# Kernel tuning notes

Measured on AMD Instinct MI355X. Metric: run time of the kernel, lower is better.

## Reference

```python
import jax, jax.numpy as jnp
import numpy as np

N_NODES = 50000
IN_CH = 128
HID = 32
HEADS = 4
OUT_CH = 32
N_EDGES = 1600000
NEG_SLOPE = 0.2


def _gatv2(x, src, dst, Wl, bl, Wr, br, att, bias, H, C):
    """GATv2Conv (PyG semantics, add_self_loops already applied to src/dst).
    x: [N, F_in]; src/dst: [E]; Wl/Wr: [F_in, H*C]; att: [H, C]; bias: [H*C].
    Returns [N, H*C] (concat heads)."""
    N = x.shape[0]
    xl = (x @ Wl + bl).reshape(N, H, C)  # source-side transform
    xr = (x @ Wr + br).reshape(N, H, C)  # target-side transform
    e = jax.nn.leaky_relu(xl[src] + xr[dst], NEG_SLOPE)  # [E, H, C]
    logits = jnp.einsum('ehc,hc->eh', e, att)  # [E, H]
    # softmax over incoming edges of each target node (stable)
    m = jax.ops.segment_max(logits, dst, num_segments=N)[dst]
    p = jnp.exp(logits - m)
    denom = jax.ops.segment_sum(p, dst, num_segments=N)[dst]
    alpha = p / denom  # [E, H]
    out = jax.ops.segment_sum(alpha[:, :, None] * xl[src], dst, num_segments=N)
    return out.reshape(N, H * C) + bias


def setup_inputs() -> dict:
    key = jax.random.key(0)
    ks = jax.random.split(key, 16)
    s1 = 1.0 / np.sqrt(IN_CH)
    s2 = 1.0 / np.sqrt(HID * HEADS)
    inp = {
        'x': jax.random.normal(ks[0], (N_NODES, IN_CH), jnp.float32),
        'edge_index': jax.random.randint(ks[1], (2, N_EDGES), 0, N_NODES, jnp.int64 if jax.config.read('jax_enable_x64') else jnp.int32).astype(jnp.int32),
        # layer 1: in -> HID per head, HEADS heads
        'Wl1': jax.random.normal(ks[2], (IN_CH, HEADS * HID), jnp.float32) * s1,
        'bl1': jnp.zeros((HEADS * HID,), jnp.float32),
        'Wr1': jax.random.normal(ks[3], (IN_CH, HEADS * HID), jnp.float32) * s1,
        'br1': jnp.zeros((HEADS * HID,), jnp.float32),
        'att1': jax.random.normal(ks[4], (HEADS, HID), jnp.float32) * s1,
        'b1': jnp.zeros((HEADS * HID,), jnp.float32),
        # mu head: HID*HEADS -> OUT_CH, 1 head
        'Wl_mu': jax.random.normal(ks[5], (HEADS * HID, OUT_CH), jnp.float32) * s2,
        'bl_mu': jnp.zeros((OUT_CH,), jnp.float32),
        'Wr_mu': jax.random.normal(ks[6], (HEADS * HID, OUT_CH), jnp.float32) * s2,
        'br_mu': jnp.zeros((OUT_CH,), jnp.float32),
        'att_mu': jax.random.normal(ks[7], (1, OUT_CH), jnp.float32) * s2,
        'b_mu': jnp.zeros((OUT_CH,), jnp.float32),
        # logvar head
        'Wl_lv': jax.random.normal(ks[8], (HEADS * HID, OUT_CH), jnp.float32) * s2,
        'bl_lv': jnp.zeros((OUT_CH,), jnp.float32),
        'Wr_lv': jax.random.normal(ks[9], (HEADS * HID, OUT_CH), jnp.float32) * s2,
        'br_lv': jnp.zeros((OUT_CH,), jnp.float32),
        'att_lv': jax.random.normal(ks[10], (1, OUT_CH), jnp.float32) * s2,
        'b_lv': jnp.zeros((OUT_CH,), jnp.float32),
    }
    return inp


def reference(x, edge_index, Wl1, bl1, Wr1, br1, att1, b1,
              Wl_mu, bl_mu, Wr_mu, br_mu, att_mu, b_mu,
              Wl_lv, bl_lv, Wr_lv, br_lv, att_lv, b_lv):
    N = x.shape[0]
    loops = jnp.arange(N, dtype=edge_index.dtype)
    src = jnp.concatenate([edge_index[0], loops])  # add_self_loops=True
    dst = jnp.concatenate([edge_index[1], loops])
    h = jax.nn.relu(_gatv2(x, src, dst, Wl1, bl1, Wr1, br1, att1, b1, HEADS, HID))
    mu = _gatv2(h, src, dst, Wl_mu, bl_mu, Wr_mu, br_mu, att_mu, b_mu, 1, OUT_CH)
    logvar = _gatv2(h, src, dst, Wl_lv, bl_lv, Wr_lv, br_lv, att_lv, b_lv, 1, OUT_CH)
    return (mu, logvar)
```

## Files before the change

kernel.cpp:

```cpp
#include <hip/hip_runtime.h>
#include <hip/hip_fp16.h>

#define NNODES 50000
#define EORIG  1600000
#define ETOT   (EORIG + NNODES)
#define NEG 0.2f
#define BSH 7
#define NBUCK ((NNODES + 127) >> BSH)
#define BCAP 5120
#define NRT (NNODES / 16)
#define EPB 4096
#define NBE ((ETOT + EPB - 1) / EPB)
#define LOG2E 1.44269504f

typedef _Float16 v2h __attribute__((ext_vector_type(2)));
typedef _Float16 v8h __attribute__((ext_vector_type(8)));
typedef float    v4f __attribute__((ext_vector_type(4)));

__device__ __forceinline__ float hdot2v(v2h a, v2h b, float c) {
#if __has_builtin(__builtin_amdgcn_fdot2)
    return __builtin_amdgcn_fdot2(a, b, c, false);
#else
    return c + (float)a.x * (float)b.x + (float)a.y * (float)b.y;
#endif
}

__device__ __forceinline__ float fexp2(float t) {
#if __has_builtin(__builtin_amdgcn_exp2f)
    return __builtin_amdgcn_exp2f(t);
#else
    return exp2f(t);
#endif
}

__global__ __launch_bounds__(256) void prep_kernel(
    const int* __restrict__ src, const int* __restrict__ dst,
    int* __restrict__ bcur, unsigned int* __restrict__ pairs,
    const float* __restrict__ Wl, const float* __restrict__ Wr,
    const float* __restrict__ Wlmu, const float* __restrict__ Wllv,
    const float* __restrict__ Wrmu, const float* __restrict__ Wrlv,
    __half* __restrict__ WT, __half* __restrict__ WT2)
{
    if (blockIdx.x >= NBE) {
        int id = (blockIdx.x - NBE) * 256 + threadIdx.x;
        if (id < 32768) {
            int k = id >> 8, c = id & 255;
            float v = (c < 128) ? Wl[k * 128 + c] : Wr[k * 128 + (c - 128)];
            WT[c * 128 + k] = __float2half(v);
        } else if (id < 49152) {
            int loc = id - 32768;
            int k = loc >> 7, c = loc & 127;
            int sel = c >> 5, cc = c & 31;
            const float* W = sel == 0 ? Wlmu : sel == 1 ? Wllv : sel == 2 ? Wrmu : Wrlv;
            WT2[c * 128 + k] = __float2half(W[k * 32 + cc]);
        }
        return;
    }

    __shared__ int cnt[NBUCK];
    __shared__ int gbase[NBUCK];
    const int e0 = blockIdx.x * EPB;

    for (int i = threadIdx.x; i < NBUCK; i += 256) cnt[i] = 0;
    __syncthreads();

    for (int i = threadIdx.x; i < EPB; i += 256) {
        int e = e0 + i;
        if (e >= ETOT) break;
        int d = (e < EORIG) ? dst[e] : e - EORIG;
        atomicAdd(&cnt[d >> BSH], 1);
    }
    __syncthreads();

    for (int b = threadIdx.x; b < NBUCK; b += 256) {
        int c = cnt[b];
        gbase[b] = c ? (b * BCAP + atomicAdd(&bcur[b], c)) : 0;
        cnt[b] = 0;
    }
    __syncthreads();

    for (int i = threadIdx.x; i < EPB; i += 256) {
        int e = e0 + i;
        if (e >= ETOT) break;
        int s, d;
        if (e < EORIG) { s = src[e]; d = dst[e]; }
        else           { s = d = e - EORIG; }
        int b = d >> BSH;
        int slot = atomicAdd(&cnt[b], 1);
        pairs[gbase[b] + slot] = (unsigned)s | ((unsigned)(d & 127) << 16);
    }
}

__global__ __launch_bounds__(256) void csrfill_kernel(
    const unsigned int* __restrict__ pairs, const int* __restrict__ bcur,
    int2* __restrict__ begend, unsigned short* __restrict__ csr)
{
    __shared__ int cnt[128];
    __shared__ int lofs[128];
    __shared__ int scnt[128];
    const int b = blockIdx.x, n0 = b << BSH;
    const int nn = min(128, NNODES - n0);
    const int pbase = b * BCAP;
    const int pend = pbase + bcur[b];
    const int t = threadIdx.x;

    if (t < 128) { cnt[t] = 0; scnt[t] = 0; }
    __syncthreads();
    for (int i = pbase + t; i < pend; i += 256)
        atomicAdd(&cnt[pairs[i] >> 16], 1);
    __syncthreads();

    int myc = (t < 128) ? cnt[t] : 0;
    if (t < 128) lofs[t] = myc;
    __syncthreads();
    for (int off = 1; off < 128; off <<= 1) {
        int v = (t < 128 && t >= off) ? lofs[t - off] : 0;
        __syncthreads();
        if (t < 128) lofs[t] += v;
        __syncthreads();
    }
    if (t < 128) lofs[t] = pbase + lofs[t] - myc;
    __syncthreads();

    if (t < nn) begend[n0 + t] = make_int2(lofs[t], lofs[t] + myc);

    for (int i = pbase + t; i < pend; i += 256) {
        unsigned pr = pairs[i];
        int l = pr >> 16;
        int slot = atomicAdd(&scnt[l], 1);
        csr[lofs[l] + slot] = (unsigned short)(pr & 0xFFFFu);
    }
}

__global__ __launch_bounds__(256) void lin1_kernel(
    const float* __restrict__ x, const __half* __restrict__ WT,
    const float* __restrict__ bl, const float* __restrict__ br,
    __half* __restrict__ xl16, __half* __restrict__ xr16)
{
    int rt = (blockIdx.x * 256 + threadIdx.x) >> 6;
    if (rt >= NRT) return;
    int l  = threadIdx.x & 63;
    int lr = l & 15, lg = l >> 4;
    int row = rt * 16 + lr;

    v8h a[4];
    const float4* xrow = reinterpret_cast<const float4*>(x + (size_t)row * 128);
    #pragma unroll
    for (int ks = 0; ks < 4; ++ks) {
        float4 f0 = xrow[ks * 8 + lg * 2];
        float4 f1 = xrow[ks * 8 + lg * 2 + 1];
        v8h t;
        t[0]=(_Float16)f0.x; t[1]=(_Float16)f0.y; t[2]=(_Float16)f0.z; t[3]=(_Float16)f0.w;
        t[4]=(_Float16)f1.x; t[5]=(_Float16)f1.y; t[6]=(_Float16)f1.z; t[7]=(_Float16)f1.w;
        a[ks] = t;
    }

    const uint4* wt4 = reinterpret_cast<const uint4*>(WT);
    #pragma unroll 4
    for (int ct = 0; ct < 16; ++ct) {
        int c = ct * 16 + lr;
        v4f acc = {0.f, 0.f, 0.f, 0.f};
        #pragma unroll
        for (int ks = 0; ks < 4; ++ks) {
            union { uint4 u; v8h h; } B;
            B.u = wt4[(size_t)c * 16 + ks * 4 + lg];
            acc = __builtin_amdgcn_mfma_f32_16x16x32_f16(a[ks], B.h, acc, 0, 0, 0);
        }
        float bb = (c < 128) ? bl[c] : br[c - 128];
        #pragma unroll
        for (int j = 0; j < 4; ++j) {
            int orow = rt * 16 + lg * 4 + j;
            __half hv = __float2half(acc[j] + bb);
            if (c < 128) xl16[(size_t)orow * 128 + c] = hv;
            else         xr16[(size_t)orow * 128 + (c - 128)] = hv;
        }
    }
}

__global__ __launch_bounds__(256) void lin2_kernel(
    const __half* __restrict__ h16, const __half* __restrict__ WT2,
    const float* __restrict__ blmu, const float* __restrict__ bllv,
    const float* __restrict__ brmu, const float* __restrict__ brlv,
    __half* __restrict__ xi16, __half* __restrict__ xrI16)
{
    int rt = (blockIdx.x * 256 + threadIdx.x) >> 6;
    if (rt >= NRT) return;
    int l  = threadIdx.x & 63;
    int lr = l & 15, lg = l >> 4;
    int row = rt * 16 + lr;

    v8h a[4];
    const uint4* hrow = reinterpret_cast<const uint4*>(h16 + (size_t)row * 128);
    #pragma unroll
    for (int ks = 0; ks < 4; ++ks) {
        union { uint4 u; v8h h; } A;
        A.u = hrow[ks * 4 + lg];
        a[ks] = A.h;
    }

    const uint4* wt4 = reinterpret_cast<const uint4*>(WT2);
    #pragma unroll 4
    for (int ct = 0; ct < 8; ++ct) {
        int c = ct * 16 + lr;
        v4f acc = {0.f, 0.f, 0.f, 0.f};
        #pragma unroll
        for (int ks = 0; ks < 4; ++ks) {
            union { uint4 u; v8h h; } B;
            B.u = wt4[(size_t)c * 16 + ks * 4 + lg];
            acc = __builtin_amdgcn_mfma_f32_16x16x32_f16(a[ks], B.h, acc, 0, 0, 0);
        }
        int sel = c >> 5, cc = c & 31;
        const float* bp = sel == 0 ? blmu : sel == 1 ? bllv : sel == 2 ? brmu : brlv;
        float bb = bp[cc];
        #pragma unroll
        for (int j = 0; j < 4; ++j) {
            int orow = rt * 16 + lg * 4 + j;
            __half hv = __float2half(acc[j] + bb);
            if (c < 64) xi16 [(size_t)orow * 64 + c]      = hv;
            else        xrI16[(size_t)orow * 64 + (c-64)] = hv;
        }
    }
}

__global__ __launch_bounds__(256) void gat_gather1(
    const __half* __restrict__ xl16, const __half* __restrict__ xr16,
    const float* __restrict__ att, const float* __restrict__ bias,
    const int2* __restrict__ begend, const unsigned short* __restrict__ csr,
    __half* __restrict__ h16)
{
    int d = (blockIdx.x * 256 + threadIdx.x) >> 6;
    if (d >= NNODES) return;
    int lane = threadIdx.x & 63;
    int quarter = lane >> 4;
    int q = lane & 15;
    int qo = quarter * 2;

    v2h xrh[4], ath[4];
    {
        union { uint4 u; v2h v[4]; } R;
        R.u = reinterpret_cast<const uint4*>(xr16)[d * 16 + q];
        #pragma unroll
        for (int j = 0; j < 4; ++j) xrh[j] = R.v[j];
        const float4* t4 = reinterpret_cast<const float4*>(att) + q * 2;
        float4 a = t4[0], b = t4[1];
        ath[0] = (v2h){(_Float16)(a.x*LOG2E), (_Float16)(a.y*LOG2E)};
        ath[1] = (v2h){(_Float16)(a.z*LOG2E), (_Float16)(a.w*LOG2E)};
        ath[2] = (v2h){(_Float16)(b.x*LOG2E), (_Float16)(b.y*LOG2E)};
        ath[3] = (v2h){(_Float16)(b.z*LOG2E), (_Float16)(b.w*LOG2E)};
    }
    const v2h neg2 = (v2h){(_Float16)NEG, (_Float16)NEG};

    int2 be = begend[d];
    int beg = be.x, end = be.y;
    int deg = end - beg;
    int nF = deg >> 3;
    int rem = deg & 7;
    const uint4* xlu = reinterpret_cast<const uint4*>(xl16);

    float den = 0.f;
    float acc[8] = {0.f,0.f,0.f,0.f,0.f,0.f,0.f,0.f};

    auto computeU = [&](uint4 U) {
        union { uint4 u; v2h v[4]; } X; X.u = U;
        float t = 0.f;
        #pragma unroll
        for (int j = 0; j < 4; ++j) {
            v2h s = X.v[j] + xrh[j];
            v2h l = __builtin_elementwise_max(s, s * neg2);
            t = hdot2v(l, ath[j], t);
        }
        t += __shfl_xor(t, 1, 64);
        t += __shfl_xor(t, 2, 64);
        float p = fexp2(t);
        den += p;
        #pragma unroll
        for (int j = 0; j < 4; ++j) {
            acc[2*j]   += p * (float)X.v[j].x;
            acc[2*j+1] += p * (float)X.v[j].y;
        }
    };
    auto computeM = [&](uint4 U, bool val) {
        union { uint4 u; v2h v[4]; } X; X.u = U;
        float t = 0.f;
        #pragma unroll
        for (int j = 0; j < 4; ++j) {
            v2h s = X.v[j] + xrh[j];
            v2h l = __builtin_elementwise_max(s, s * neg2);
            t = hdot2v(l, ath[j], t);
        }
        t += __shfl_xor(t, 1, 64);
        t += __shfl_xor(t, 2, 64);
        float p = val ? fexp2(t) : 0.f;
        den += p;
        #pragma unroll
        for (int j = 0; j < 4; ++j) {
            acc[2*j]   += p * (float)X.v[j].x;
            acc[2*j+1] += p * (float)X.v[j].y;
        }
    };

    int iA0 = csr[beg + qo],     iA1 = csr[beg + qo + 1];
    uint4 rA0 = xlu[iA0 * 16 + q], rA1 = xlu[iA1 * 16 + q];
    int iB0 = csr[beg + 8 + qo], iB1 = csr[beg + 8 + qo + 1];

    for (int it = 0; it < nF; ++it) {
        int b2 = beg + (it + 2) * 8;
        int iC0 = csr[b2 + qo], iC1 = csr[b2 + qo + 1];
        uint4 rB0 = xlu[iB0 * 16 + q];
        uint4 rB1 = xlu[iB1 * 16 + q];
        computeU(rA0);
        computeU(rA1);
        rA0 = rB0; rA1 = rB1;
        iB0 = iC0; iB1 = iC1;
    }
    if (rem) {
        computeM(rA0, qo < rem);
        computeM(rA1, qo + 1 < rem);
    }

    den += __shfl_xor(den, 16, 64);
    den += __shfl_xor(den, 32, 64);
    #pragma unroll
    for (int j = 0; j < 8; ++j) {
        acc[j] += __shfl_xor(acc[j], 16, 64);
        acc[j] += __shfl_xor(acc[j], 32, 64);
    }

    if (quarter == 0) {
        float r = 1.f / den;
        const float4* bp = reinterpret_cast<const float4*>(bias) + q * 2;
        float4 ba = bp[0], bb = bp[1];
        __half hv[8];
        hv[0] = __float2half(fmaxf(acc[0]*r+ba.x, 0.f));
        hv[1] = __float2half(fmaxf(acc[1]*r+ba.y, 0.f));
        hv[2] = __float2half(fmaxf(acc[2]*r+ba.z, 0.f));
        hv[3] = __float2half(fmaxf(acc[3]*r+ba.w, 0.f));
        hv[4] = __float2half(fmaxf(acc[4]*r+bb.x, 0.f));
        hv[5] = __float2half(fmaxf(acc[5]*r+bb.y, 0.f));
        hv[6] = __float2half(fmaxf(acc[6]*r+bb.z, 0.f));
        hv[7] = __float2half(fmaxf(acc[7]*r+bb.w, 0.f));
        *reinterpret_cast<uint4*>(&h16[(size_t)d * 128 + q * 8]) =
            *reinterpret_cast<uint4*>(hv);
    }
}

__global__ __launch_bounds__(256) void gat_gather2(
    const __half* __restrict__ xi16, const __half* __restrict__ xrI16,
    const float* __restrict__ atmu, const float* __restrict__ atlv,
    const float* __restrict__ bmu,  const float* __restrict__ blv,
    const int2* __restrict__ begend, const unsigned short* __restrict__ csr,
    float* __restrict__ out)
{
    int d = (blockIdx.x * 256 + threadIdx.x) >> 6;
    if (d >= NNODES) return;
    int lane = threadIdx.x & 63;
    int oct = lane >> 3;
    int r   = lane & 7;
    bool lv = r >= 4;
    int cq  = lv ? r - 4 : r;

    v2h xrh[4], ath[4];
    {
        union { uint4 u; v2h v[4]; } R;
        R.u = reinterpret_cast<const uint4*>(xrI16)[d * 8 + r];
        #pragma unroll
        for (int j = 0; j < 4; ++j) xrh[j] = R.v[j];
        const float4* t4 = reinterpret_cast<const float4*>(lv ? atlv : atmu) + cq * 2;
        float4 a = t4[0], b = t4[1];
        ath[0] = (v2h){(_Float16)(a.x*LOG2E), (_Float16)(a.y*LOG2E)};
        ath[1] = (v2h){(_Float16)(a.z*LOG2E), (_Float16)(a.w*LOG2E)};
        ath[2] = (v2h){(_Float16)(b.x*LOG2E), (_Float16)(b.y*LOG2E)};
        ath[3] = (v2h){(_Float16)(b.z*LOG2E), (_Float16)(b.w*LOG2E)};
    }
    const v2h neg2 = (v2h){(_Float16)NEG, (_Float16)NEG};

    int2 be = begend[d];
    int beg = be.x, end = be.y;
    int deg = end - beg;
    int nF = deg >> 3;
    int rem = deg & 7;
    const uint4* xiu = reinterpret_cast<const uint4*>(xi16);

    float den = 0.f;
    float acc[8] = {0.f,0.f,0.f,0.f,0.f,0.f,0.f,0.f};

    auto computeU = [&](uint4 U) {
        union { uint4 u; v2h v[4]; } X; X.u = U;
        float t = 0.f;
        #pragma unroll
        for (int j = 0; j < 4; ++j) {
            v2h s = X.v[j] + xrh[j];
            v2h l = __builtin_elementwise_max(s, s * neg2);
            t = hdot2v(l, ath[j], t);
        }
        t += __shfl_xor(t, 1, 64);
        t += __shfl_xor(t, 2, 64);
        float p = fexp2(t);
        den += p;
        #pragma unroll
        for (int j = 0; j < 4; ++j) {
            acc[2*j]   += p * (float)X.v[j].x;
            acc[2*j+1] += p * (float)X.v[j].y;
        }
    };
    auto computeM = [&](uint4 U, bool val) {
        union { uint4 u; v2h v[4]; } X; X.u = U;
        float t = 0.f;
        #pragma unroll
        for (int j = 0; j < 4; ++j) {
            v2h s = X.v[j] + xrh[j];
            v2h l = __builtin_elementwise_max(s, s * neg2);
            t = hdot2v(l, ath[j], t);
        }
        t += __shfl_xor(t, 1, 64);
        t += __shfl_xor(t, 2, 64);
        float p = val ? fexp2(t) : 0.f;
        den += p;
        #pragma unroll
        for (int j = 0; j < 4; ++j) {
            acc[2*j]   += p * (float)X.v[j].x;
            acc[2*j+1] += p * (float)X.v[j].y;
        }
    };

    int iA = csr[beg + oct];
    uint4 rA = xiu[iA * 8 + r];
    int iB = csr[beg + 8 + oct];

    for (int it = 0; it < nF; ++it) {
        int iC = csr[beg + (it + 2) * 8 + oct];
        uint4 rB = xiu[iB * 8 + r];
        computeU(rA);
        rA = rB; iB = iC;
    }
    if (rem) computeM(rA, oct < rem);

    den += __shfl_xor(den, 8, 64);
    den += __shfl_xor(den, 16, 64);
    den += __shfl_xor(den, 32, 64);
    #pragma unroll
    for (int j = 0; j < 8; ++j) {
        acc[j] += __shfl_xor(acc[j], 8, 64);
        acc[j] += __shfl_xor(acc[j], 16, 64);
        acc[j] += __shfl_xor(acc[j], 32, 64);
    }

    if (oct == 0) {
        float rr = 1.f / den;
        const float4* bp = reinterpret_cast<const float4*>(lv ? blv : bmu) + cq * 2;
        float4 ba = bp[0], bb = bp[1];
        float4 o1 = make_float4(acc[0]*rr+ba.x, acc[1]*rr+ba.y,
                                acc[2]*rr+ba.z, acc[3]*rr+ba.w);
        float4 o2 = make_float4(acc[4]*rr+bb.x, acc[5]*rr+bb.y,
                                acc[6]*rr+bb.z, acc[7]*rr+bb.w);
        float* base_out = out + (lv ? 1600000 : 0);
        float4* op = reinterpret_cast<float4*>(base_out) + (size_t)d * 8 + cq * 2;
        op[0] = o1; op[1] = o2;
    }
}

extern "C" void kernel_launch(void* const* d_in, const int* in_sizes, int n_in,
                              void* d_out, int out_size, void* d_ws, size_t ws_size,
                              hipStream_t stream) {
    const float* x    = (const float*)d_in[0];
    const int*   ei   = (const int*)d_in[1];
    const float* Wl1  = (const float*)d_in[2];
    const float* bl1  = (const float*)d_in[3];
    const float* Wr1  = (const float*)d_in[4];
    const float* br1  = (const float*)d_in[5];
    const float* att1 = (const float*)d_in[6];
    const float* b1   = (const float*)d_in[7];
    const float* Wlmu = (const float*)d_in[8];
    const float* blmu = (const float*)d_in[9];
    const float* Wrmu = (const float*)d_in[10];
    const float* brmu = (const float*)d_in[11];
    const float* atmu = (const float*)d_in[12];
    const float* bmu  = (const float*)d_in[13];
    const float* Wllv = (const float*)d_in[14];
    const float* bllv = (const float*)d_in[15];
    const float* Wrlv = (const float*)d_in[16];
    const float* brlv = (const float*)d_in[17];
    const float* atlv = (const float*)d_in[18];
    const float* blv  = (const float*)d_in[19];

    float* out = (float*)d_out;
    float* ws  = (float*)d_ws;

    __half* xl16 = (__half*)ws;
    __half* xr16 = (__half*)(ws + 3200000);
    __half* h16  = (__half*)(ws + 6400000);
    __half* WT   = (__half*)(ws + 9600000);
    __half* WT2  = (__half*)(ws + 9620000);

    __half* xi16  = (__half*)ws;
    __half* xrI16 = (__half*)(ws + 1600000);

    int* ip = (int*)(ws + 10000000);
    unsigned int*   pairs  = (unsigned int*)ip;
    int*            bcur   = ip + 2001920;
    int2*           begend = (int2*)(ip + 2002312);
    unsigned short* csr    = (unsigned short*)(ip + 2102312);

    const int* srcp = ei;
    const int* dstp = ei + EORIG;

    hipMemsetAsync(bcur, 0, NBUCK * sizeof(int), stream);
    prep_kernel<<<NBE + 192, 256, 0, stream>>>(
        srcp, dstp, bcur, pairs, Wl1, Wr1, Wlmu, Wllv, Wrmu, Wrlv, WT, WT2);
    csrfill_kernel<<<NBUCK, 256, 0, stream>>>(pairs, bcur, begend, csr);

    lin1_kernel<<<(NRT + 3) / 4, 256, 0, stream>>>(x, WT, bl1, br1, xl16, xr16);

    gat_gather1<<<(NNODES * 64 + 255) / 256, 256, 0, stream>>>(
        xl16, xr16, att1, b1, begend, csr, h16);

    lin2_kernel<<<(NRT + 3) / 4, 256, 0, stream>>>(
        h16, WT2, blmu, bllv, brmu, brlv, xi16, xrI16);

    gat_gather2<<<(NNODES * 64 + 255) / 256, 256, 0, stream>>>(
        xi16, xrI16, atmu, atlv, bmu, blv, begend, csr, out);
}
```

Before: 199.7 us.

## Fuse CSR fill with lin1 launch and process two edges per lane in gather2

Merges the CSR fill kernel and the first linear transform into one launch, with block index selecting the role. The two are independent, so they can run concurrently and one launch disappears. In gat_gather2, each octet of lanes now handles two edges per iteration (16 edges per step) with masked tail handling through clamped indices. This doubles the loads in flight per lane and drops the separate remainder path, at the cost of more registers and some wasted work on the padded tail.

Result: faster. 187.5 us (-6.1%).

```diff
diff --git a/kernel.cpp b/kernel.cpp
--- a/kernel.cpp
+++ b/kernel.cpp
@@ -9,6 +9,7 @@
 #define NBUCK ((NNODES + 127) >> BSH)
 #define BCAP 5120
 #define NRT (NNODES / 16)
+#define NLB ((NRT + 3) / 4)
 #define EPB 4096
 #define NBE ((ETOT + EPB - 1) / EPB)
 #define LOG2E 1.44269504f
@@ -91,53 +92,53 @@
     }
 }
 
-__global__ __launch_bounds__(256) void csrfill_kernel(
+__global__ __launch_bounds__(256) void fill_lin1_kernel(
     const unsigned int* __restrict__ pairs, const int* __restrict__ bcur,
-    int2* __restrict__ begend, unsigned short* __restrict__ csr)
-{
-    __shared__ int cnt[128];
-    __shared__ int lofs[128];
-    __shared__ int scnt[128];
-    const int b = blockIdx.x, n0 = b << BSH;
-    const int nn = min(128, NNODES - n0);
-    const int pbase = b * BCAP;
-    const int pend = pbase + bcur[b];
-    const int t = threadIdx.x;
-
-    if (t < 128) { cnt[t] = 0; scnt[t] = 0; }
-    __syncthreads();
-    for (int i = pbase + t; i < pend; i += 256)
-        atomicAdd(&cnt[pairs[i] >> 16], 1);
-    __syncthreads();
-
-    int myc = (t < 128) ? cnt[t] : 0;
-    if (t < 128) lofs[t] = myc;
-    __syncthreads();
-    for (int off = 1; off < 128; off <<= 1) {
-        int v = (t < 128 && t >= off) ? lofs[t - off] : 0;
-        __syncthreads();
-        if (t < 128) lofs[t] += v;
-        __syncthreads();
-    }
-    if (t < 128) lofs[t] = pbase + lofs[t] - myc;
-    __syncthreads();
-
-    if (t < nn) begend[n0 + t] = make_int2(lofs[t], lofs[t] + myc);
-
-    for (int i = pbase + t; i < pend; i += 256) {
-        unsigned pr = pairs[i];
-        int l = pr >> 16;
-        int slot = atomicAdd(&scnt[l], 1);
-        csr[lofs[l] + slot] = (unsigned short)(pr & 0xFFFFu);
-    }
-}
-
-__global__ __launch_bounds__(256) void lin1_kernel(
+    int2* __restrict__ begend, unsigned short* __restrict__ csr,
     const float* __restrict__ x, const __half* __restrict__ WT,
     const float* __restrict__ bl, const float* __restrict__ br,
     __half* __restrict__ xl16, __half* __restrict__ xr16)
 {
-    int rt = (blockIdx.x * 256 + threadIdx.x) >> 6;
+    if (blockIdx.x < NBUCK) {
+        __shared__ int cnt[128];
+        __shared__ int lofs[128];
+        __shared__ int scnt[128];
+        const int b = blockIdx.x, n0 = b << BSH;
+        const int nn = min(128, NNODES - n0);
+        const int pbase = b * BCAP;
+        const int pend = pbase + bcur[b];
+        const int t = threadIdx.x;
+
+        if (t < 128) { cnt[t] = 0; scnt[t] = 0; }
+        __syncthreads();
+        for (int i = pbase + t; i < pend; i += 256)
+            atomicAdd(&cnt[pairs[i] >> 16], 1);
+        __syncthreads();
+
+        int myc = (t < 128) ? cnt[t] : 0;
+        if (t < 128) lofs[t] = myc;
+        __syncthreads();
+        for (int off = 1; off < 128; off <<= 1) {
+            int v = (t < 128 && t >= off) ? lofs[t - off] : 0;
+            __syncthreads();
+            if (t < 128) lofs[t] += v;
+            __syncthreads();
+        }
+        if (t < 128) lofs[t] = pbase + lofs[t] - myc;
+        __syncthreads();
+
+        if (t < nn) begend[n0 + t] = make_int2(lofs[t], lofs[t] + myc);
+
+        for (int i = pbase + t; i < pend; i += 256) {
+            unsigned pr = pairs[i];
+            int l = pr >> 16;
+            int slot = atomicAdd(&scnt[l], 1);
+            csr[lofs[l] + slot] = (unsigned short)(pr & 0xFFFFu);
+        }
+        return;
+    }
+
+    int rt = ((blockIdx.x - NBUCK) * 256 + threadIdx.x) >> 6;
     if (rt >= NRT) return;
     int l  = threadIdx.x & 63;
     int lr = l & 15, lg = l >> 4;
@@ -358,6 +359,7 @@
     int r   = lane & 7;
     bool lv = r >= 4;
     int cq  = lv ? r - 4 : r;
+    int oo = oct * 2;
 
     v2h xrh[4], ath[4];
     {
@@ -376,34 +378,13 @@
 
     int2 be = begend[d];
     int beg = be.x, end = be.y;
-    int deg = end - beg;
-    int nF = deg >> 3;
-    int rem = deg & 7;
+    int nI = (end - beg + 15) >> 4;
     const uint4* xiu = reinterpret_cast<const uint4*>(xi16);
 
     float den = 0.f;
     float acc[8] = {0.f,0.f,0.f,0.f,0.f,0.f,0.f,0.f};
 
-    auto computeU = [&](uint4 U) {
-        union { uint4 u; v2h v[4]; } X; X.u = U;
-        float t = 0.f;
-        #pragma unroll
-        for (int j = 0; j < 4; ++j) {
-            v2h s = X.v[j] + xrh[j];
-            v2h l = __builtin_elementwise_max(s, s * neg2);
-            t = hdot2v(l, ath[j], t);
-        }
-        t += __shfl_xor(t, 1, 64);
-        t += __shfl_xor(t, 2, 64);
-        float p = fexp2(t);
-        den += p;
-        #pragma unroll
-        for (int j = 0; j < 4; ++j) {
-            acc[2*j]   += p * (float)X.v[j].x;
-            acc[2*j+1] += p * (float)X.v[j].y;
-        }
-    };
-    auto computeM = [&](uint4 U, bool val) {
+    auto compute = [&](uint4 U, bool val) {
         union { uint4 u; v2h v[4]; } X; X.u = U;
         float t = 0.f;
         #pragma unroll
@@ -423,17 +404,45 @@
         }
     };
 
-    int iA = csr[beg + oct];
-    uint4 rA = xiu[iA * 8 + r];
-    int iB = csr[beg + 8 + oct];
-
-    for (int it = 0; it < nF; ++it) {
-        int iC = csr[beg + (it + 2) * 8 + oct];
-        uint4 rB = xiu[iB * 8 + r];
-        computeU(rA);
-        rA = rB; iB = iC;
-    }
-    if (rem) computeM(rA, oct < rem);
+    int  iA[2], iB[2];
+    bool vA[2], vB[2];
+    uint4 rA[2];
+
+    #pragma unroll
+    for (int k = 0; k < 2; ++k) {
+        int s = beg + oo + k;
+        vA[k] = s < end;
+        iA[k] = csr[vA[k] ? s : end - 1];
+    }
+    #pragma unroll
+    for (int k = 0; k < 2; ++k) rA[k] = xiu[iA[k] * 8 + r];
+    #pragma unroll
+    for (int k = 0; k < 2; ++k) {
+        int s = beg + 16 + oo + k;
+        vB[k] = s < end;
+        iB[k] = csr[vB[k] ? s : end - 1];
+    }
+
+    for (int it = 0; it < nI; ++it) {
+        int b2 = beg + (it + 2) * 16;
+        int  iC[2]; bool vC[2];
+        #pragma unroll
+        for (int k = 0; k < 2; ++k) {
+            int s = b2 + oo + k;
+            vC[k] = s < end;
+            iC[k] = csr[vC[k] ? s : end - 1];
+        }
+        uint4 rB[2];
+        #pragma unroll
+        for (int k = 0; k < 2; ++k) rB[k] = xiu[iB[k] * 8 + r];
+        #pragma unroll
+        for (int k = 0; k < 2; ++k) compute(rA[k], vA[k]);
+        #pragma unroll
+        for (int k = 0; k < 2; ++k) {
+            rA[k] = rB[k]; vA[k] = vB[k];
+            iB[k] = iC[k]; vB[k] = vC[k];
+        }
+    }
 
     den += __shfl_xor(den, 8, 64);
     den += __shfl_xor(den, 16, 64);
@@ -507,9 +516,9 @@
     hipMemsetAsync(bcur, 0, NBUCK * sizeof(int), stream);
     prep_kernel<<<NBE + 192, 256, 0, stream>>>(
         srcp, dstp, bcur, pairs, Wl1, Wr1, Wlmu, Wllv, Wrmu, Wrlv, WT, WT2);
-    csrfill_kernel<<<NBUCK, 256, 0, stream>>>(pairs, bcur, begend, csr);
-
-    lin1_kernel<<<(NRT + 3) / 4, 256, 0, stream>>>(x, WT, bl1, br1, xl16, xr16);
+
+    fill_lin1_kernel<<<NBUCK + NLB, 256, 0, stream>>>(
+        pairs, bcur, begend, csr, x, WT, bl1, br1, xl16, xr16);
 
     gat_gather1<<<(NNODES * 64 + 255) / 256, 256, 0, stream>>>(
         xl16, xr16, att1, b1, begend, csr, h16);
```
